# Performance work log

Measured on AMD Instinct MI355X. Metric: run time of the kernel, lower is better.

## Reference

```python
import jax, jax.numpy as jnp
import numpy as np

N, E, D = 100000, 1600000, 128

def setup_inputs() -> dict:
    key = jax.random.key(0)
    ks = jax.random.split(key, 8)
    s = 1.0 / np.sqrt(D)
    return {
        "x": jax.random.normal(ks[0], (N, D), dtype=jnp.float32),
        "edge_index": jax.random.randint(ks[1], (2, E), 0, N, dtype=jnp.int64),
        "Wl0": jax.random.uniform(ks[2], (D, D), jnp.float32, -s, s),
        "Wr0": jax.random.uniform(ks[3], (D, D), jnp.float32, -s, s),
        "b0": jnp.zeros((D,), jnp.float32),
        "Wl1": jax.random.uniform(ks[4], (D, D), jnp.float32, -s, s),
        "Wr1": jax.random.uniform(ks[5], (D, D), jnp.float32, -s, s),
        "b1": jnp.zeros((D,), jnp.float32),
    }

def reference(x, edge_index, Wl0, Wr0, b0, Wl1, Wr1, b1):
    # SAGEConv (mean aggr, root_weight=True): out = mean_{j in N(i)} h_j @ Wl + h_i @ Wr + b
    src, dst = edge_index[0], edge_index[1]
    n = x.shape[0]
    # in-degree counts for mean aggregation (clamped to avoid div-by-zero)
    cnt = jax.ops.segment_sum(jnp.ones((src.shape[0],), x.dtype), dst, num_segments=n)
    denom = jnp.maximum(cnt, 1.0)[:, None]  # [N,1]

    def sage_layer(h, Wl, Wr, b):
        agg = jax.ops.segment_sum(h[src], dst, num_segments=n) / denom  # [N,D]
        # norm='none', dropout inactive at inference -> just relu
        return jax.nn.relu(agg @ Wl + h @ Wr + b)

    h = sage_layer(x, Wl0, Wr0, b0)
    h = sage_layer(h, Wl1, Wr1, b1)
    return h
```

## Files before the change

kernel.cpp:

```cpp
#include <hip/hip_runtime.h>
#include <hip/hip_bf16.h>


#define D 128
#define WSTRIDE 136
#define WPANEL (D * WSTRIDE)
#define GCAP 12288

typedef __attribute__((ext_vector_type(8))) short short8v;
typedef __attribute__((ext_vector_type(4))) float f32x4;

__device__ inline unsigned short f2bf(float f) {
  unsigned u = __float_as_uint(f);
  return (unsigned short)((u + 0x7FFFu + ((u >> 16) & 1u)) >> 16);
}
__device__ inline unsigned pack2(float lo, float hi) {
  return (unsigned)f2bf(lo) | ((unsigned)f2bf(hi) << 16);
}


__global__ __launch_bounds__(256) void k_bin(const int* __restrict__ ei, int E,
                                             int* __restrict__ gcur,
                                             int* __restrict__ gbuf) {
  __shared__ int hcnt[256], hbase[256], hfill[256];
  int tid = threadIdx.x;
  hcnt[tid] = 0;
  __syncthreads();
  int ent[8], bk[8];
#pragma unroll
  for (int it = 0; it < 8; ++it) {
    int e = blockIdx.x * 2048 + it * 256 + tid;
    if (e < E) {
      int s = ei[e], d = ei[E + e];
      bk[it] = d >> 9;
      ent[it] = (s << 9) | (d & 511);
      atomicAdd(&hcnt[bk[it]], 1);
    } else bk[it] = -1;
  }
  __syncthreads();
  int c = hcnt[tid];
  hbase[tid] = c ? atomicAdd(&gcur[tid], c) : 0;
  hfill[tid] = 0;
  __syncthreads();
#pragma unroll
  for (int it = 0; it < 8; ++it) {
    if (bk[it] >= 0) {
      int slot = atomicAdd(&hfill[bk[it]], 1);
      gbuf[(size_t)bk[it] * GCAP + hbase[bk[it]] + slot] = ent[it];
    }
  }
}


__global__ __launch_bounds__(256) void k_hist(const int* __restrict__ gcur,
                                              const int* __restrict__ gbuf,
                                              int* __restrict__ cnt, int n) {
  __shared__ int hc[512];
  int b = blockIdx.x, tid = threadIdx.x;
  hc[tid] = 0; hc[tid + 256] = 0;
  __syncthreads();
  int m = gcur[b];
  for (int i = tid; i < m; i += 256)
    atomicAdd(&hc[gbuf[(size_t)b * GCAP + i] & 511], 1);
  __syncthreads();
#pragma unroll
  for (int k = 0; k < 2; ++k) {
    int i = k * 256 + tid, node = b * 512 + i;
    if (node < n) cnt[node] = hc[i];
  }
}


__global__ __launch_bounds__(1024) void k_scan1(const int* __restrict__ cnt, int n,
                                                int* __restrict__ rowptr,
                                                float* __restrict__ inv_denom,
                                                int* __restrict__ bsum) {
  __shared__ int wsum[16];
  int tid = threadIdx.x, lane = tid & 63, wid = tid >> 6;
  int i = blockIdx.x * 1024 + tid;
  int v = (i < n) ? cnt[i] : 0;
  int x = v;
#pragma unroll
  for (int off = 1; off < 64; off <<= 1) {
    int t = __shfl_up(x, (unsigned)off);
    if (lane >= off) x += t;
  }
  if (lane == 63) wsum[wid] = x;
  __syncthreads();
  if (tid < 16) {
    int w = wsum[tid], y = w;
#pragma unroll
    for (int off = 1; off < 16; off <<= 1) {
      int t = __shfl_up(y, (unsigned)off);
      if (tid >= off) y += t;
    }
    wsum[tid] = y - w;
  }
  __syncthreads();
  if (i < n) {
    rowptr[i] = wsum[wid] + x - v;
    inv_denom[i] = 1.0f / (float)((v > 1) ? v : 1);
  }
  if (tid == 1023) bsum[blockIdx.x] = wsum[15] + x;
}

__global__ __launch_bounds__(64) void k_scan2(int* __restrict__ bsum, int nb,
                                              int* __restrict__ rowptr, int n) {
  int lane = threadIdx.x;
  int v0 = (lane < nb) ? bsum[lane] : 0;
  int v1 = (64 + lane < nb) ? bsum[64 + lane] : 0;
  int x = v0;
#pragma unroll
  for (int off = 1; off < 64; off <<= 1) {
    int t = __shfl_up(x, (unsigned)off);
    if (lane >= off) x += t;
  }
  int tot0 = __shfl(x, 63);
  int y = v1;
#pragma unroll
  for (int off = 1; off < 64; off <<= 1) {
    int t = __shfl_up(y, (unsigned)off);
    if (lane >= off) y += t;
  }
  if (lane < nb) bsum[lane] = x - v0;
  if (64 + lane < nb) bsum[64 + lane] = tot0 + (y - v1);
  if (lane == 63) rowptr[n] = tot0 + y;
}

__global__ __launch_bounds__(1024) void k_scan3(int* __restrict__ rowptr,
                                                const int* __restrict__ bsum, int n) {
  int i = blockIdx.x * 1024 + threadIdx.x;
  if (i < n) rowptr[i] += bsum[blockIdx.x];
}


__global__ __launch_bounds__(256) void k_place(const int* __restrict__ gcur,
                                               const int* __restrict__ gbuf,
                                               const int* __restrict__ rowptr,
                                               int* __restrict__ csr, int n) {
  __shared__ int rp[512], hf[512];
  int b = blockIdx.x, tid = threadIdx.x;
#pragma unroll
  for (int k = 0; k < 2; ++k) {
    int i = k * 256 + tid, node = b * 512 + i;
    rp[i] = (node < n) ? rowptr[node] : 0;
    hf[i] = 0;
  }
  __syncthreads();
  int m = gcur[b];
  for (int i = tid; i < m; i += 256) {
    int ent = gbuf[(size_t)b * GCAP + i];
    int d = ent & 511, s = ent >> 9;
    csr[rp[d] + atomicAdd(&hf[d], 1)] = s;
  }
}


__global__ __launch_bounds__(256) void k_tobf16(const float* __restrict__ in,
                                                short* __restrict__ ob, long long ng) {
  long long i = (long long)blockIdx.x * 256 + threadIdx.x;
  if (i >= ng) return;
  const float4* p = (const float4*)in + i * 2;
  float4 a = p[0], b = p[1];
  uint4 o;
  o.x = pack2(a.x, a.y); o.y = pack2(a.z, a.w);
  o.z = pack2(b.x, b.y); o.w = pack2(b.z, b.w);
  ((uint4*)ob)[i] = o;
}


__global__ __launch_bounds__(256) void k_wprep(const float* __restrict__ W0,
                                               const float* __restrict__ W1,
                                               const float* __restrict__ W2,
                                               const float* __restrict__ W3,
                                               short* __restrict__ WT) {
  const float* W = (blockIdx.y == 0) ? W0 : (blockIdx.y == 1) ? W1
                 : (blockIdx.y == 2) ? W2 : W3;
  short* o = WT + (size_t)blockIdx.y * WPANEL;
  int i = blockIdx.x * 256 + threadIdx.x;
  if (i < D * D) {
    int k = i >> 7, c = i & 127;
    o[c * WSTRIDE + k] = (short)f2bf(W[i]);
  }
}


__global__ __launch_bounds__(256) void k_agg_bf(const short* __restrict__ hb,
                                                const int* __restrict__ rowptr,
                                                const int* __restrict__ csr,
                                                const float* __restrict__ inv_denom,
                                                short* __restrict__ agg, int n) {
  int gw = (int)((blockIdx.x * 256u + threadIdx.x) >> 6);
  if (gw >= n) return;
  int lane = threadIdx.x & 63;
  int q = lane >> 4, s16 = lane & 15;
  int beg = __builtin_amdgcn_readfirstlane(rowptr[gw]);
  int end = __builtin_amdgcn_readfirstlane(rowptr[gw + 1]);
  float acc[8];
#pragma unroll
  for (int k = 0; k < 8; ++k) acc[k] = 0.f;
  int e = beg + q;
  for (; e + 4 < end; e += 8) {
    int s0 = csr[e], s1 = csr[e + 4];
    uint4 v0 = ((const uint4*)(hb + (size_t)s0 * D))[s16];
    uint4 v1 = ((const uint4*)(hb + (size_t)s1 * D))[s16];
    acc[0] += __uint_as_float(v0.x << 16); acc[1] += __uint_as_float(v0.x & 0xffff0000u);
    acc[2] += __uint_as_float(v0.y << 16); acc[3] += __uint_as_float(v0.y & 0xffff0000u);
    acc[4] += __uint_as_float(v0.z << 16); acc[5] += __uint_as_float(v0.z & 0xffff0000u);
    acc[6] += __uint_as_float(v0.w << 16); acc[7] += __uint_as_float(v0.w & 0xffff0000u);
    acc[0] += __uint_as_float(v1.x << 16); acc[1] += __uint_as_float(v1.x & 0xffff0000u);
    acc[2] += __uint_as_float(v1.y << 16); acc[3] += __uint_as_float(v1.y & 0xffff0000u);
    acc[4] += __uint_as_float(v1.z << 16); acc[5] += __uint_as_float(v1.z & 0xffff0000u);
    acc[6] += __uint_as_float(v1.w << 16); acc[7] += __uint_as_float(v1.w & 0xffff0000u);
  }
  if (e < end) {
    int s0 = csr[e];
    uint4 v0 = ((const uint4*)(hb + (size_t)s0 * D))[s16];
    acc[0] += __uint_as_float(v0.x << 16); acc[1] += __uint_as_float(v0.x & 0xffff0000u);
    acc[2] += __uint_as_float(v0.y << 16); acc[3] += __uint_as_float(v0.y & 0xffff0000u);
    acc[4] += __uint_as_float(v0.z << 16); acc[5] += __uint_as_float(v0.z & 0xffff0000u);
    acc[6] += __uint_as_float(v0.w << 16); acc[7] += __uint_as_float(v0.w & 0xffff0000u);
  }
#pragma unroll
  for (int k = 0; k < 8; ++k) {
    acc[k] += __shfl_xor(acc[k], 16);
    acc[k] += __shfl_xor(acc[k], 32);
  }
  if (q == 0) {
    float iv = inv_denom[gw];
    uint4 o;
    o.x = pack2(acc[0] * iv, acc[1] * iv);
    o.y = pack2(acc[2] * iv, acc[3] * iv);
    o.z = pack2(acc[4] * iv, acc[5] * iv);
    o.w = pack2(acc[6] * iv, acc[7] * iv);
    ((uint4*)(agg + (size_t)gw * D))[s16] = o;
  }
}


template <int OUTF>
__global__ __launch_bounds__(512) void k_fgemm_bf(const short* __restrict__ A,
                                                  const short* __restrict__ H,
                                                  const short* __restrict__ WTl,
                                                  const short* __restrict__ WTr,
                                                  const float* __restrict__ bias,
                                                  void* __restrict__ outv, int n) {
  __shared__ short wl[WPANEL];
  __shared__ short wr[WPANEL];
  int tid = threadIdx.x;
  for (int i = tid; i < WPANEL / 8; i += 512) {
    ((int4*)wl)[i] = ((const int4*)WTl)[i];
    ((int4*)wr)[i] = ((const int4*)WTr)[i];
  }
  __syncthreads();

  int lane = tid & 63, wid = tid >> 6;
  int c = lane & 15, g = lane >> 4;
  float bv[8];
#pragma unroll
  for (int cc = 0; cc < 8; ++cc) bv[cc] = bias[cc * 16 + c];

  int ntile = (n + 15) >> 4;
  for (int tile = blockIdx.x * 8 + wid; tile < ntile; tile += gridDim.x * 8) {
    int r0 = tile * 16;
    int row = r0 + c;
    bool rok = row < n;
    f32x4 acc[8];
#pragma unroll
    for (int cc = 0; cc < 8; ++cc) acc[cc] = (f32x4){0.f, 0.f, 0.f, 0.f};

#pragma unroll
    for (int t = 0; t < 4; ++t) {
      short8v af = (short8v){0,0,0,0,0,0,0,0};
      short8v hf = (short8v){0,0,0,0,0,0,0,0};
      if (rok) {
        af = *(const short8v*)(A + (size_t)row * D + t * 32 + g * 8);
        hf = *(const short8v*)(H + (size_t)row * D + t * 32 + g * 8);
      }
      int kb = t * 32 + g * 8;
#pragma unroll
      for (int cc = 0; cc < 8; ++cc) {
        short8v bl = *(const short8v*)&wl[(cc * 16 + c) * WSTRIDE + kb];
        acc[cc] = __builtin_amdgcn_mfma_f32_16x16x32_bf16(af, bl, acc[cc], 0, 0, 0);
        short8v br = *(const short8v*)&wr[(cc * 16 + c) * WSTRIDE + kb];
        acc[cc] = __builtin_amdgcn_mfma_f32_16x16x32_bf16(hf, br, acc[cc], 0, 0, 0);
      }
    }
#pragma unroll
    for (int cc = 0; cc < 8; ++cc) {
#pragma unroll
      for (int i = 0; i < 4; ++i) {
        int rr = r0 + g * 4 + i;
        if (rr < n) {
          float o = acc[cc][i] + bv[cc];
          o = o > 0.f ? o : 0.f;
          if (OUTF) ((float*)outv)[(size_t)rr * D + cc * 16 + c] = o;
          else ((short*)outv)[(size_t)rr * D + cc * 16 + c] = (short)f2bf(o);
        }
      }
    }
  }
}


__global__ __launch_bounds__(256) void k_agg_f32(const float* __restrict__ h,
                                                 const int* __restrict__ rowptr,
                                                 const int* __restrict__ csr,
                                                 const float* __restrict__ inv_denom,
                                                 float* __restrict__ agg, int n) {
  int gw = (int)((blockIdx.x * 256u + threadIdx.x) >> 6);
  if (gw >= n) return;
  int lane = threadIdx.x & 63;
  int half = lane >> 5, sub = lane & 31;
  int beg = __builtin_amdgcn_readfirstlane(rowptr[gw]);
  int end = __builtin_amdgcn_readfirstlane(rowptr[gw + 1]);
  float sx0 = 0.f, sy0 = 0.f, sz0 = 0.f, sw0 = 0.f;
  float sx1 = 0.f, sy1 = 0.f, sz1 = 0.f, sw1 = 0.f;
  int e = beg;
  for (; e + 4 <= end; e += 4) {
    int i0 = csr[e + half];
    int i1 = csr[e + 2 + half];
    float4 v0 = ((const float4*)(h + (size_t)i0 * D))[sub];
    float4 v1 = ((const float4*)(h + (size_t)i1 * D))[sub];
    sx0 += v0.x; sy0 += v0.y; sz0 += v0.z; sw0 += v0.w;
    sx1 += v1.x; sy1 += v1.y; sz1 += v1.z; sw1 += v1.w;
  }
  if (e + 2 <= end) {
    int i0 = csr[e + half];
    float4 v0 = ((const float4*)(h + (size_t)i0 * D))[sub];
    sx0 += v0.x; sy0 += v0.y; sz0 += v0.z; sw0 += v0.w;
    e += 2;
  }
  if (e < end) {
    int i0 = csr[e];
    float4 v0 = ((const float4*)(h + (size_t)i0 * D))[sub];
    if (half == 0) { sx0 += v0.x; sy0 += v0.y; sz0 += v0.z; sw0 += v0.w; }
  }
  float sx = sx0 + sx1, sy = sy0 + sy1, sz = sz0 + sz1, sw = sw0 + sw1;
  sx += __shfl_xor(sx, 32); sy += __shfl_xor(sy, 32);
  sz += __shfl_xor(sz, 32); sw += __shfl_xor(sw, 32);
  if (half == 0) {
    float iv = inv_denom[gw];
    float4 r; r.x = sx * iv; r.y = sy * iv; r.z = sz * iv; r.w = sw * iv;
    ((float4*)(agg + (size_t)gw * D))[sub] = r;
  }
}

__global__ __launch_bounds__(512) void k_fgemm_f32(const float* A, const float* H,
                                                   const short* __restrict__ WTl,
                                                   const short* __restrict__ WTr,
                                                   const float* __restrict__ bias,
                                                   float* out, int n) {
  __shared__ short wl[WPANEL];
  __shared__ short wr[WPANEL];
  int tid = threadIdx.x;
  for (int i = tid; i < WPANEL / 8; i += 512) {
    ((int4*)wl)[i] = ((const int4*)WTl)[i];
    ((int4*)wr)[i] = ((const int4*)WTr)[i];
  }
  __syncthreads();
  int lane = tid & 63, wid = tid >> 6;
  int c = lane & 15, g = lane >> 4;
  float bv[8];
#pragma unroll
  for (int cc = 0; cc < 8; ++cc) bv[cc] = bias[cc * 16 + c];
  int ntile = (n + 15) >> 4;
  for (int tile = blockIdx.x * 8 + wid; tile < ntile; tile += gridDim.x * 8) {
    int r0 = tile * 16;
    int row = r0 + c;
    bool rok = row < n;
    f32x4 acc[8];
#pragma unroll
    for (int cc = 0; cc < 8; ++cc) acc[cc] = (f32x4){0.f, 0.f, 0.f, 0.f};
#pragma unroll
    for (int t = 0; t < 4; ++t) {
      short8v af = (short8v){0,0,0,0,0,0,0,0};
      short8v hf = (short8v){0,0,0,0,0,0,0,0};
      if (rok) {
        const float4* pa = (const float4*)(A + (size_t)row * D + t * 32 + g * 8);
        float4 a0 = pa[0], a1 = pa[1];
        const float4* ph = (const float4*)(H + (size_t)row * D + t * 32 + g * 8);
        float4 h0 = ph[0], h1 = ph[1];
        af[0] = (short)f2bf(a0.x); af[1] = (short)f2bf(a0.y); af[2] = (short)f2bf(a0.z); af[3] = (short)f2bf(a0.w);
        af[4] = (short)f2bf(a1.x); af[5] = (short)f2bf(a1.y); af[6] = (short)f2bf(a1.z); af[7] = (short)f2bf(a1.w);
        hf[0] = (short)f2bf(h0.x); hf[1] = (short)f2bf(h0.y); hf[2] = (short)f2bf(h0.z); hf[3] = (short)f2bf(h0.w);
        hf[4] = (short)f2bf(h1.x); hf[5] = (short)f2bf(h1.y); hf[6] = (short)f2bf(h1.z); hf[7] = (short)f2bf(h1.w);
      }
      int kb = t * 32 + g * 8;
#pragma unroll
      for (int cc = 0; cc < 8; ++cc) {
        short8v bl = *(const short8v*)&wl[(cc * 16 + c) * WSTRIDE + kb];
        acc[cc] = __builtin_amdgcn_mfma_f32_16x16x32_bf16(af, bl, acc[cc], 0, 0, 0);
        short8v br = *(const short8v*)&wr[(cc * 16 + c) * WSTRIDE + kb];
        acc[cc] = __builtin_amdgcn_mfma_f32_16x16x32_bf16(hf, br, acc[cc], 0, 0, 0);
      }
    }
#pragma unroll
    for (int cc = 0; cc < 8; ++cc) {
#pragma unroll
      for (int i = 0; i < 4; ++i) {
        int rr = r0 + g * 4 + i;
        if (rr < n) {
          float o = acc[cc][i] + bv[cc];
          out[(size_t)rr * D + cc * 16 + c] = o > 0.f ? o : 0.f;
        }
      }
    }
  }
}


extern "C" void kernel_launch(void* const* d_in, const int* in_sizes, int n_in,
                              void* d_out, int out_size, void* d_ws, size_t ws_size,
                              hipStream_t stream) {
  const float* x   = (const float*)d_in[0];
  const int*   ei  = (const int*)d_in[1];
  const float* Wl0 = (const float*)d_in[2];
  const float* Wr0 = (const float*)d_in[3];
  const float* b0  = (const float*)d_in[4];
  const float* Wl1 = (const float*)d_in[5];
  const float* Wr1 = (const float*)d_in[6];
  const float* b1  = (const float*)d_in[7];
  const int N = in_sizes[0] / D;
  const int E = in_sizes[1] / 2;
  float* out = (float*)d_out;

  size_t NP = ((size_t)N + 64) & ~(size_t)63;
  size_t EP = ((size_t)E + 63) & ~(size_t)63;
  const int NBUCK = (N + 511) >> 9;

  int* W = (int*)d_ws;
  size_t off = 0;
  int*   rowptr = W + off; off += NP;
  int*   cnt    = W + off; off += NP;
  float* inv    = (float*)(W + off); off += NP;
  int*   bsum   = W + off; off += 1024;
  int*   gcur   = W + off; off += 256;
  int*   csr    = W + off; off += EP;
  short* wt     = (short*)(W + off); off += (size_t)4 * WPANEL / 2;
  size_t base = off;
  short* aggb = (short*)(W + off); off += NP * 64;
  short* xb   = (short*)(W + off); off += NP * 64;
  short* h1b  = (short*)(W + off); off += NP * 64;
  size_t need_new = off * 4;
  float* aggf = (float*)(W + base);
  bool use_bf = ws_size >= need_new;
  int* gbuf = use_bf ? (int*)xb : (int*)aggf;

  hipMemsetAsync(gcur, 0, 256 * sizeof(int), stream);

  int NB = (N + 1023) / 1024;
  k_bin<<<(E + 2047) / 2048, 256, 0, stream>>>(ei, E, gcur, gbuf);
  k_hist<<<NBUCK, 256, 0, stream>>>(gcur, gbuf, cnt, N);
  k_scan1<<<NB, 1024, 0, stream>>>(cnt, N, rowptr, inv, bsum);
  k_scan2<<<1, 64, 0, stream>>>(bsum, NB, rowptr, N);
  k_scan3<<<NB, 1024, 0, stream>>>(rowptr, bsum, N);
  k_place<<<NBUCK, 256, 0, stream>>>(gcur, gbuf, rowptr, csr, N);

  dim3 wgrid((D * D + 255) / 256, 4);
  k_wprep<<<wgrid, 256, 0, stream>>>(Wl0, Wr0, Wl1, Wr1, wt);

  int agrid = (N + 3) / 4;

  if (use_bf) {
    long long ng = (long long)N * (D / 8);
    k_tobf16<<<(int)((ng + 255) / 256), 256, 0, stream>>>(x, xb, ng);
    k_agg_bf<<<agrid, 256, 0, stream>>>(xb, rowptr, csr, inv, aggb, N);
    k_fgemm_bf<0><<<512, 512, 0, stream>>>(aggb, xb, wt, wt + WPANEL, b0, h1b, N);
    k_agg_bf<<<agrid, 256, 0, stream>>>(h1b, rowptr, csr, inv, aggb, N);
    k_fgemm_bf<1><<<512, 512, 0, stream>>>(aggb, h1b, wt + 2 * WPANEL, wt + 3 * WPANEL, b1, out, N);
  } else {
    k_agg_f32<<<agrid, 256, 0, stream>>>(x, rowptr, csr, inv, aggf, N);
    k_fgemm_f32<<<512, 512, 0, stream>>>(aggf, x, wt, wt + WPANEL, b0, out, N);
    k_agg_f32<<<agrid, 256, 0, stream>>>(out, rowptr, csr, inv, aggf, N);
    k_fgemm_f32<<<512, 512, 0, stream>>>(aggf, out, wt + 2 * WPANEL, wt + 3 * WPANEL, b1, out, N);
  }
}
```

Baseline: 319.4 us.

## Stage GEMM epilogue through LDS for coalesced row stores; one tile per wave

The fused SAGE GEMM epilogue now writes bias+ReLU results into a per-wave LDS staging buffer. It then emits whole output rows as 16-byte vector stores, replacing the scattered 2- or 4-byte per-element global writes. The grid is also resized so each wave handles exactly one 16-row tile instead of using a fixed 512 persistent blocks. The cost is extra LDS (up to 64KB more for the fp32 output path), which may reduce occupancy, and each block now reloads the weight panels for only one tile per wave.

```diff
diff --git a/kernel.cpp b/kernel.cpp
--- a/kernel.cpp
+++ b/kernel.cpp
@@ -247,6 +247,10 @@
                                                   void* __restrict__ outv, int n) {
   __shared__ short wl[WPANEL];
   __shared__ short wr[WPANEL];
+  constexpr int SSTR = OUTF ? 132 : 136;
+  constexpr int SBYTES = 8 * 16 * SSTR * (OUTF ? 4 : 2);
+  __shared__ int4 stageraw[SBYTES / 16];
+
   int tid = threadIdx.x;
   for (int i = tid; i < WPANEL / 8; i += 512) {
     ((int4*)wl)[i] = ((const int4*)WTl)[i];
@@ -259,6 +263,8 @@
   float bv[8];
 #pragma unroll
   for (int cc = 0; cc < 8; ++cc) bv[cc] = bias[cc * 16 + c];
+
+  int srow = lane >> 2, sch = lane & 3;
 
   int ntile = (n + 15) >> 4;
   for (int tile = blockIdx.x * 8 + wid; tile < ntile; tile += gridDim.x * 8) {
@@ -286,17 +292,36 @@
         acc[cc] = __builtin_amdgcn_mfma_f32_16x16x32_bf16(hf, br, acc[cc], 0, 0, 0);
       }
     }
-#pragma unroll
-    for (int cc = 0; cc < 8; ++cc) {
-#pragma unroll
-      for (int i = 0; i < 4; ++i) {
-        int rr = r0 + g * 4 + i;
-        if (rr < n) {
+
+    if (OUTF) {
+      float* st = (float*)stageraw + (size_t)wid * 16 * SSTR;
+#pragma unroll
+      for (int cc = 0; cc < 8; ++cc)
+#pragma unroll
+        for (int i = 0; i < 4; ++i) {
           float o = acc[cc][i] + bv[cc];
-          o = o > 0.f ? o : 0.f;
-          if (OUTF) ((float*)outv)[(size_t)rr * D + cc * 16 + c] = o;
-          else ((short*)outv)[(size_t)rr * D + cc * 16 + c] = (short)f2bf(o);
+          st[(g * 4 + i) * SSTR + cc * 16 + c] = o > 0.f ? o : 0.f;
         }
+      if (r0 + srow < n) {
+        const float4* src = (const float4*)(st + srow * SSTR + sch * 32);
+        float4* dst = (float4*)((float*)outv + (size_t)(r0 + srow) * D + sch * 32);
+#pragma unroll
+        for (int j = 0; j < 8; ++j) dst[j] = src[j];
+      }
+    } else {
+      short* st = (short*)stageraw + (size_t)wid * 16 * SSTR;
+#pragma unroll
+      for (int cc = 0; cc < 8; ++cc)
+#pragma unroll
+        for (int i = 0; i < 4; ++i) {
+          float o = acc[cc][i] + bv[cc];
+          st[(g * 4 + i) * SSTR + cc * 16 + c] = (short)f2bf(o > 0.f ? o : 0.f);
+        }
+      if (r0 + srow < n) {
+        const int4* src = (const int4*)(st + srow * SSTR + sch * 32);
+        int4* dst = (int4*)((short*)outv + (size_t)(r0 + srow) * D + sch * 32);
+#pragma unroll
+        for (int j = 0; j < 4; ++j) dst[j] = src[j];
       }
     }
   }
@@ -461,14 +486,15 @@
   k_wprep<<<wgrid, 256, 0, stream>>>(Wl0, Wr0, Wl1, Wr1, wt);
 
   int agrid = (N + 3) / 4;
+  int ggrid = ((N + 15) / 16 + 7) / 8;
 
   if (use_bf) {
     long long ng = (long long)N * (D / 8);
     k_tobf16<<<(int)((ng + 255) / 256), 256, 0, stream>>>(x, xb, ng);
     k_agg_bf<<<agrid, 256, 0, stream>>>(xb, rowptr, csr, inv, aggb, N);
-    k_fgemm_bf<0><<<512, 512, 0, stream>>>(aggb, xb, wt, wt + WPANEL, b0, h1b, N);
+    k_fgemm_bf<0><<<ggrid, 512, 0, stream>>>(aggb, xb, wt, wt + WPANEL, b0, h1b, N);
     k_agg_bf<<<agrid, 256, 0, stream>>>(h1b, rowptr, csr, inv, aggb, N);
-    k_fgemm_bf<1><<<512, 512, 0, stream>>>(aggb, h1b, wt + 2 * WPANEL, wt + 3 * WPANEL, b1, out, N);
+    k_fgemm_bf<1><<<ggrid, 512, 0, stream>>>(aggb, h1b, wt + 2 * WPANEL, wt + 3 * WPANEL, b1, out, N);
   } else {
     k_agg_f32<<<agrid, 256, 0, stream>>>(x, rowptr, csr, inv, aggf, N);
     k_fgemm_f32<<<512, 512, 0, stream>>>(aggf, x, wt, wt + WPANEL, b0, out, N);
```

Result: slower. 373.8 us (+17.0%).

## Pre-swizzle weights into MFMA fragment layout and load them directly from global memory

Applied to the files above, without the earlier changes.

Weights are pre-packed into the exact per-lane MFMA B-fragment order, so the fused GEMM reads them with coalesced global/L2 loads instead of staging 68KB of LDS panels per block behind a barrier. Each wave now processes 32 rows (two 16-row tiles) so every weight fragment feeds four MFMAs, and the grid is sized to one tile per wave instead of a persistent loop. The gather-aggregation loop is also unrolled to issue four neighbour-row loads per iteration for more memory-level parallelism. The tradeoff is repeated weight reads through cache for every wave and many more small blocks.

```diff
diff --git a/kernel.cpp b/kernel.cpp
--- a/kernel.cpp
+++ b/kernel.cpp
@@ -166,6 +166,24 @@
   o.x = pack2(a.x, a.y); o.y = pack2(a.z, a.w);
   o.z = pack2(b.x, b.y); o.w = pack2(b.z, b.w);
   ((uint4*)ob)[i] = o;
+}
+
+
+__global__ __launch_bounds__(256) void k_wprep_frag(const float* __restrict__ W0,
+                                                    const float* __restrict__ W1,
+                                                    const float* __restrict__ W2,
+                                                    const float* __restrict__ W3,
+                                                    short* __restrict__ WF) {
+  const float* W = (blockIdx.y == 0) ? W0 : (blockIdx.y == 1) ? W1
+                 : (blockIdx.y == 2) ? W2 : W3;
+  short* o = WF + (size_t)blockIdx.y * (D * D);
+  int i = blockIdx.x * 256 + threadIdx.x;
+  if (i < D * D) {
+    int j = i & 7, l = (i >> 3) & 63, cc = (i >> 9) & 7, t = i >> 12;
+    int k = t * 32 + (l >> 4) * 8 + j;
+    int c = cc * 16 + (l & 15);
+    o[i] = (short)f2bf(W[k * D + c]);
+  }
 }
 
 
@@ -199,27 +217,31 @@
   float acc[8];
 #pragma unroll
   for (int k = 0; k < 8; ++k) acc[k] = 0.f;
+  auto addrow = [&](uint4 v) {
+    acc[0] += __uint_as_float(v.x << 16); acc[1] += __uint_as_float(v.x & 0xffff0000u);
+    acc[2] += __uint_as_float(v.y << 16); acc[3] += __uint_as_float(v.y & 0xffff0000u);
+    acc[4] += __uint_as_float(v.z << 16); acc[5] += __uint_as_float(v.z & 0xffff0000u);
+    acc[6] += __uint_as_float(v.w << 16); acc[7] += __uint_as_float(v.w & 0xffff0000u);
+  };
   int e = beg + q;
+  for (; e + 12 < end; e += 16) {
+    int s0 = csr[e], s1 = csr[e + 4], s2 = csr[e + 8], s3 = csr[e + 12];
+    uint4 v0 = ((const uint4*)(hb + (size_t)s0 * D))[s16];
+    uint4 v1 = ((const uint4*)(hb + (size_t)s1 * D))[s16];
+    uint4 v2 = ((const uint4*)(hb + (size_t)s2 * D))[s16];
+    uint4 v3 = ((const uint4*)(hb + (size_t)s3 * D))[s16];
+    addrow(v0); addrow(v1); addrow(v2); addrow(v3);
+  }
   for (; e + 4 < end; e += 8) {
     int s0 = csr[e], s1 = csr[e + 4];
     uint4 v0 = ((const uint4*)(hb + (size_t)s0 * D))[s16];
     uint4 v1 = ((const uint4*)(hb + (size_t)s1 * D))[s16];
-    acc[0] += __uint_as_float(v0.x << 16); acc[1] += __uint_as_float(v0.x & 0xffff0000u);
-    acc[2] += __uint_as_float(v0.y << 16); acc[3] += __uint_as_float(v0.y & 0xffff0000u);
-    acc[4] += __uint_as_float(v0.z << 16); acc[5] += __uint_as_float(v0.z & 0xffff0000u);
-    acc[6] += __uint_as_float(v0.w << 16); acc[7] += __uint_as_float(v0.w & 0xffff0000u);
-    acc[0] += __uint_as_float(v1.x << 16); acc[1] += __uint_as_float(v1.x & 0xffff0000u);
-    acc[2] += __uint_as_float(v1.y << 16); acc[3] += __uint_as_float(v1.y & 0xffff0000u);
-    acc[4] += __uint_as_float(v1.z << 16); acc[5] += __uint_as_float(v1.z & 0xffff0000u);
-    acc[6] += __uint_as_float(v1.w << 16); acc[7] += __uint_as_float(v1.w & 0xffff0000u);
+    addrow(v0); addrow(v1);
   }
   if (e < end) {
     int s0 = csr[e];
     uint4 v0 = ((const uint4*)(hb + (size_t)s0 * D))[s16];
-    acc[0] += __uint_as_float(v0.x << 16); acc[1] += __uint_as_float(v0.x & 0xffff0000u);
-    acc[2] += __uint_as_float(v0.y << 16); acc[3] += __uint_as_float(v0.y & 0xffff0000u);
-    acc[4] += __uint_as_float(v0.z << 16); acc[5] += __uint_as_float(v0.z & 0xffff0000u);
-    acc[6] += __uint_as_float(v0.w << 16); acc[7] += __uint_as_float(v0.w & 0xffff0000u);
+    addrow(v0);
   }
 #pragma unroll
   for (int k = 0; k < 8; ++k) {
@@ -239,64 +261,75 @@
 
 
 template <int OUTF>
-__global__ __launch_bounds__(512) void k_fgemm_bf(const short* __restrict__ A,
+__global__ __launch_bounds__(256) void k_fgemm_bf(const short* __restrict__ A,
                                                   const short* __restrict__ H,
-                                                  const short* __restrict__ WTl,
-                                                  const short* __restrict__ WTr,
+                                                  const short* __restrict__ WFl,
+                                                  const short* __restrict__ WFr,
                                                   const float* __restrict__ bias,
                                                   void* __restrict__ outv, int n) {
-  __shared__ short wl[WPANEL];
-  __shared__ short wr[WPANEL];
   int tid = threadIdx.x;
-  for (int i = tid; i < WPANEL / 8; i += 512) {
-    ((int4*)wl)[i] = ((const int4*)WTl)[i];
-    ((int4*)wr)[i] = ((const int4*)WTr)[i];
-  }
-  __syncthreads();
-
-  int lane = tid & 63, wid = tid >> 6;
+  int lane = tid & 63, w4 = tid >> 6;
+  int nt = (n + 31) >> 5;
+  int wtile = blockIdx.x * 4 + w4;
+  if (wtile >= nt) return;
   int c = lane & 15, g = lane >> 4;
+  int r0 = wtile * 32;
+  int row0 = r0 + c, row1 = r0 + 16 + c;
+  bool ok0 = row0 < n, ok1 = row1 < n;
+
   float bv[8];
 #pragma unroll
   for (int cc = 0; cc < 8; ++cc) bv[cc] = bias[cc * 16 + c];
 
-  int ntile = (n + 15) >> 4;
-  for (int tile = blockIdx.x * 8 + wid; tile < ntile; tile += gridDim.x * 8) {
-    int r0 = tile * 16;
-    int row = r0 + c;
-    bool rok = row < n;
-    f32x4 acc[8];
-#pragma unroll
-    for (int cc = 0; cc < 8; ++cc) acc[cc] = (f32x4){0.f, 0.f, 0.f, 0.f};
-
-#pragma unroll
-    for (int t = 0; t < 4; ++t) {
-      short8v af = (short8v){0,0,0,0,0,0,0,0};
-      short8v hf = (short8v){0,0,0,0,0,0,0,0};
-      if (rok) {
-        af = *(const short8v*)(A + (size_t)row * D + t * 32 + g * 8);
-        hf = *(const short8v*)(H + (size_t)row * D + t * 32 + g * 8);
-      }
-      int kb = t * 32 + g * 8;
-#pragma unroll
-      for (int cc = 0; cc < 8; ++cc) {
-        short8v bl = *(const short8v*)&wl[(cc * 16 + c) * WSTRIDE + kb];
-        acc[cc] = __builtin_amdgcn_mfma_f32_16x16x32_bf16(af, bl, acc[cc], 0, 0, 0);
-        short8v br = *(const short8v*)&wr[(cc * 16 + c) * WSTRIDE + kb];
-        acc[cc] = __builtin_amdgcn_mfma_f32_16x16x32_bf16(hf, br, acc[cc], 0, 0, 0);
-      }
+  const short8v* Fl = (const short8v*)WFl;
+  const short8v* Fr = (const short8v*)WFr;
+
+  f32x4 acc0[8], acc1[8];
+#pragma unroll
+  for (int cc = 0; cc < 8; ++cc) {
+    acc0[cc] = (f32x4){0.f, 0.f, 0.f, 0.f};
+    acc1[cc] = (f32x4){0.f, 0.f, 0.f, 0.f};
+  }
+
+#pragma unroll
+  for (int t = 0; t < 4; ++t) {
+    short8v a0 = (short8v){0,0,0,0,0,0,0,0}, h0 = a0, a1 = a0, h1 = a0;
+    int kb = t * 32 + g * 8;
+    if (ok0) {
+      a0 = *(const short8v*)(A + (size_t)row0 * D + kb);
+      h0 = *(const short8v*)(H + (size_t)row0 * D + kb);
+    }
+    if (ok1) {
+      a1 = *(const short8v*)(A + (size_t)row1 * D + kb);
+      h1 = *(const short8v*)(H + (size_t)row1 * D + kb);
     }
 #pragma unroll
     for (int cc = 0; cc < 8; ++cc) {
-#pragma unroll
-      for (int i = 0; i < 4; ++i) {
-        int rr = r0 + g * 4 + i;
-        if (rr < n) {
-          float o = acc[cc][i] + bv[cc];
-          o = o > 0.f ? o : 0.f;
-          if (OUTF) ((float*)outv)[(size_t)rr * D + cc * 16 + c] = o;
-          else ((short*)outv)[(size_t)rr * D + cc * 16 + c] = (short)f2bf(o);
-        }
+      short8v bl = Fl[(t * 8 + cc) * 64 + lane];
+      short8v br = Fr[(t * 8 + cc) * 64 + lane];
+      acc0[cc] = __builtin_amdgcn_mfma_f32_16x16x32_bf16(a0, bl, acc0[cc], 0, 0, 0);
+      acc0[cc] = __builtin_amdgcn_mfma_f32_16x16x32_bf16(h0, br, acc0[cc], 0, 0, 0);
+      acc1[cc] = __builtin_amdgcn_mfma_f32_16x16x32_bf16(a1, bl, acc1[cc], 0, 0, 0);
+      acc1[cc] = __builtin_amdgcn_mfma_f32_16x16x32_bf16(h1, br, acc1[cc], 0, 0, 0);
+    }
+  }
+
+#pragma unroll
+  for (int cc = 0; cc < 8; ++cc) {
+#pragma unroll
+    for (int i = 0; i < 4; ++i) {
+      int rr0 = r0 + g * 4 + i;
+      int rr1 = rr0 + 16;
+      float o0 = acc0[cc][i] + bv[cc];
+      float o1 = acc1[cc][i] + bv[cc];
+      o0 = o0 > 0.f ? o0 : 0.f;
+      o1 = o1 > 0.f ? o1 : 0.f;
+      if (OUTF) {
+        if (rr0 < n) ((float*)outv)[(size_t)rr0 * D + cc * 16 + c] = o0;
+        if (rr1 < n) ((float*)outv)[(size_t)rr1 * D + cc * 16 + c] = o1;
+      } else {
+        if (rr0 < n) ((short*)outv)[(size_t)rr0 * D + cc * 16 + c] = (short)f2bf(o0);
+        if (rr1 < n) ((short*)outv)[(size_t)rr1 * D + cc * 16 + c] = (short)f2bf(o1);
       }
     }
   }
@@ -438,6 +471,7 @@
   int*   gcur   = W + off; off += 256;
   int*   csr    = W + off; off += EP;
   short* wt     = (short*)(W + off); off += (size_t)4 * WPANEL / 2;
+  short* wf     = (short*)(W + off); off += (size_t)4 * (D * D) / 2;
   size_t base = off;
   short* aggb = (short*)(W + off); off += NP * 64;
   short* xb   = (short*)(W + off); off += NP * 64;
@@ -457,19 +491,21 @@
   k_scan3<<<NB, 1024, 0, stream>>>(rowptr, bsum, N);
   k_place<<<NBUCK, 256, 0, stream>>>(gcur, gbuf, rowptr, csr, N);
 
+  int agrid = (N + 3) / 4;
   dim3 wgrid((D * D + 255) / 256, 4);
-  k_wprep<<<wgrid, 256, 0, stream>>>(Wl0, Wr0, Wl1, Wr1, wt);
-
-  int agrid = (N + 3) / 4;
 
   if (use_bf) {
+    k_wprep_frag<<<wgrid, 256, 0, stream>>>(Wl0, Wr0, Wl1, Wr1, wf);
     long long ng = (long long)N * (D / 8);
     k_tobf16<<<(int)((ng + 255) / 256), 256, 0, stream>>>(x, xb, ng);
+    int nt32 = (N + 31) >> 5;
+    int ggrid = (nt32 + 3) / 4;
     k_agg_bf<<<agrid, 256, 0, stream>>>(xb, rowptr, csr, inv, aggb, N);
-    k_fgemm_bf<0><<<512, 512, 0, stream>>>(aggb, xb, wt, wt + WPANEL, b0, h1b, N);
+    k_fgemm_bf<0><<<ggrid, 256, 0, stream>>>(aggb, xb, wf, wf + D * D, b0, h1b, N);
     k_agg_bf<<<agrid, 256, 0, stream>>>(h1b, rowptr, csr, inv, aggb, N);
-    k_fgemm_bf<1><<<512, 512, 0, stream>>>(aggb, h1b, wt + 2 * WPANEL, wt + 3 * WPANEL, b1, out, N);
+    k_fgemm_bf<1><<<ggrid, 256, 0, stream>>>(aggb, h1b, wf + 2 * D * D, wf + 3 * D * D, b1, out, N);
   } else {
+    k_wprep<<<wgrid, 256, 0, stream>>>(Wl0, Wr0, Wl1, Wr1, wt);
     k_agg_f32<<<agrid, 256, 0, stream>>>(x, rowptr, csr, inv, aggf, N);
     k_fgemm_f32<<<512, 512, 0, stream>>>(aggf, x, wt, wt + WPANEL, b0, out, N);
     k_agg_f32<<<agrid, 256, 0, stream>>>(out, rowptr, csr, inv, aggf, N);
```

Measured after the change: 263.4 us. 17.5% less time.
